# Performance work log

Measured on AMD Instinct MI355X. Metric: run time of the kernel, lower is better.

Reference implementation:

```python
import jax, jax.numpy as jnp
import numpy as np

B, T_DEC, T_ENC, E, ENC_D, VOCAB, SOS = 128, 550, 500, 512, 512, 31, 0


def setup_inputs() -> dict:
    key = jax.random.key(0)
    ks = jax.random.split(key, 16)
    s = 0.02
    d = {
        'encoder_output': jax.random.normal(ks[0], (B, T_ENC, ENC_D), jnp.float32),
        'emb': jax.random.normal(ks[1], (VOCAB, E), jnp.float32) * s,
        'w_ih0': jax.random.normal(ks[2], (4 * E, 2 * E), jnp.float32) * s,
        'w_hh0': jax.random.normal(ks[3], (4 * E, E), jnp.float32) * s,
        'b_ih0': jnp.zeros((4 * E,), jnp.float32),
        'b_hh0': jnp.zeros((4 * E,), jnp.float32),
        'w_ih1': jax.random.normal(ks[4], (4 * E, E), jnp.float32) * s,
        'w_hh1': jax.random.normal(ks[5], (4 * E, E), jnp.float32) * s,
        'b_ih1': jnp.zeros((4 * E,), jnp.float32),
        'b_hh1': jnp.zeros((4 * E,), jnp.float32),
        'wk': jax.random.normal(ks[6], (ENC_D, E), jnp.float32) * s,
        'wv': jax.random.normal(ks[7], (ENC_D, E), jnp.float32) * s,
        'w_o2c': jax.random.normal(ks[8], (E, 2 * E), jnp.float32) * s,
        'b_o2c': jnp.zeros((E,), jnp.float32),
        'b_cp': jnp.zeros((VOCAB,), jnp.float32),
    }
    return d


def _lstm_cell(x, h, c, w_ih, w_hh, b_ih, b_hh):
    # PyTorch LSTMCell gate order: i, f, g, o
    g = x @ w_ih.T + b_ih + h @ w_hh.T + b_hh
    i, f, gg, o = jnp.split(g, 4, axis=-1)
    c2 = jax.nn.sigmoid(f) * c + jax.nn.sigmoid(i) * jnp.tanh(gg)
    h2 = jax.nn.sigmoid(o) * jnp.tanh(c2)
    return h2, c2


def reference(encoder_output, emb, w_ih0, w_hh0, b_ih0, b_hh0,
              w_ih1, w_hh1, b_ih1, b_hh1, wk, wv, w_o2c, b_o2c, b_cp):
    # Precompute attention keys/values once (listener features are static)
    keys = jnp.einsum('bte,ed->btd', encoder_output, wk)    # [B,Tenc,E]
    values = jnp.einsum('bte,ed->btd', encoder_output, wv)  # [B,Tenc,E]

    z = jnp.zeros((B, E), jnp.float32)
    init = (z, z, z, z, z, jnp.full((B,), SOS, jnp.int32))

    def step(carry, _):
        h0, c0, h1, c1, ctx, sym = carry
        char_embed = emb[sym]                                # [B,E]
        x = jnp.concatenate([char_embed, ctx], axis=-1)      # [B,2E]
        h0, c0 = _lstm_cell(x, h0, c0, w_ih0, w_hh0, b_ih0, b_hh0)
        h1, c1 = _lstm_cell(h0, h1, c1, w_ih1, w_hh1, b_ih1, b_hh1)
        energy = jnp.einsum('btd,bd->bt', keys, h1)          # [B,Tenc]
        aw = jax.nn.softmax(energy, axis=-1)
        ctx = jnp.einsum('bt,btd->bd', aw, values)           # [B,E]
        cdn_in = jnp.concatenate([h1, ctx], axis=-1)         # [B,2E]
        hid = jax.nn.relu(cdn_in @ w_o2c.T + b_o2c)
        logits = hid @ emb.T + b_cp                          # [B,31] (tied weights)
        sym = jnp.argmax(logits, axis=-1).astype(jnp.int32)  # greedy feedback
        return (h0, c0, h1, c1, ctx, sym), (logits, aw)

    _, (raw, attn) = jax.lax.scan(step, init, None, length=T_DEC)
    # [T,B,...] -> [B,T,...]
    return jnp.transpose(raw, (1, 0, 2)), jnp.transpose(attn, (1, 0, 2))
```

## Files before the change

kernel.cpp:

```cpp
#include <hip/hip_runtime.h>
#include <math.h>

#define BATCH 128
#define TDEC  550
#define TENC  500
#define EDIM  512
#define VOC   31
#define NBLK  256
#define NTHR  512

#define OFF_WA   0u
#define OFF_WB   (OFF_WA + 2097152u)
#define OFF_GM   (OFF_WB + 2097152u)
#define OFF_E2G  (OFF_GM + 524288u)
#define OFF_BA   (OFF_E2G + 63488u)
#define OFF_BB   (OFF_BA + 2048u)
#define OFF_BG   (OFF_BB + 2048u)
#define OFF_ST   (OFF_BG + 512u)
#define OFF_H0T0 (OFF_ST   + 65536u)
#define OFF_H0T1 (OFF_H0T0 + 65536u)
#define OFF_H1T0 (OFF_H0T1 + 65536u)
#define OFF_H1T1 (OFF_H1T0 + 65536u)
#define OFF_C0T  (OFF_H1T1 + 65536u)
#define OFF_C1T  (OFF_C0T  + 65536u)
#define OFF_P    (OFF_C1T  + 65536u)
#define OFF_PL   (OFF_P    + 65536u)
#define OFF_PS   (OFF_PL   + 256u)
#define OFF_LB   (OFF_PS   + 131072u)
#define OFF_BAR  (OFF_LB   + 8192u)
#define OFF_WKT  (OFF_BAR  + 8192u)
#define OFF_H1BK (OFF_WKT  + 262144u)

typedef float f32x4_t __attribute__((ext_vector_type(4)));

__device__ __forceinline__ float ldv(const float* p) {
  return __hip_atomic_load((const float*)p, __ATOMIC_RELAXED, __HIP_MEMORY_SCOPE_AGENT);
}
__device__ __forceinline__ void stv(float* p, float v) {
  __hip_atomic_store(p, v, __ATOMIC_RELAXED, __HIP_MEMORY_SCOPE_AGENT);
}
__device__ __forceinline__ float4 ld_nt4(const float* p) {
  f32x4_t v = __builtin_nontemporal_load((const f32x4_t*)p);
  float4 r; r.x = v.x; r.y = v.y; r.z = v.z; r.w = v.w; return r;
}

__global__ void initCopy(const float* __restrict__ w_hh0, const float* __restrict__ w_ih1,
                         const float* __restrict__ w_hh1, const float* __restrict__ w_o2c,
                         const float* __restrict__ b_ih0, const float* __restrict__ b_hh0,
                         const float* __restrict__ b_ih1, const float* __restrict__ b_hh1,
                         const float* __restrict__ b_o2c, const float* __restrict__ wk,
                         float* __restrict__ ws)
{
  const unsigned n0 = 2048u*512u;
  const unsigned n1 = 2048u*512u;
  const unsigned n2 = 2048u*512u;
  const unsigned n3 = 512u*512u;
  const unsigned nz = 7u*65536u;
  const unsigned nw = 262144u;
  const unsigned NT = n0+n1+n2+n3 + 2048u+2048u+512u + nz + 8192u + 8192u + nw;
  for (unsigned i = blockIdx.x*blockDim.x + threadIdx.x; i < NT; i += gridDim.x*blockDim.x) {
    unsigned j = i;
    if (j < n0) { unsigned r = j & 2047u, k = j >> 11;
      ws[OFF_WA + (512u + k)*2048u + r] = w_hh0[(size_t)r*512u + k]; continue; }
    j -= n0;
    if (j < n1) { unsigned r = j & 2047u, k = j >> 11;
      ws[OFF_WB + k*2048u + r] = w_ih1[(size_t)r*512u + k]; continue; }
    j -= n1;
    if (j < n2) { unsigned r = j & 2047u, k = j >> 11;
      ws[OFF_WB + (512u + k)*2048u + r] = w_hh1[(size_t)r*512u + k]; continue; }
    j -= n2;
    if (j < n3) { unsigned r = j>>9, k = j&511u;
      ws[OFF_GM + r*1024u + k] = w_o2c[r*1024u + k]; continue; }
    j -= n3;
    if (j < 2048u) { ws[OFF_BA + j] = b_ih0[j] + b_hh0[j]; continue; }
    j -= 2048u;
    if (j < 2048u) { ws[OFF_BB + j] = b_ih1[j] + b_hh1[j]; continue; }
    j -= 2048u;
    if (j < 512u)  { ws[OFF_BG + j] = b_o2c[j]; continue; }
    j -= 512u;
    if (j < nz)    { ws[OFF_ST + j] = 0.f; continue; }
    j -= nz;
    if (j < 8192u) {
      unsigned buf = j>>12, v = j & 31u;
      ws[OFF_LB + j] = (buf==1u && v==0u) ? 1e9f : 0.f;
      continue; }
    j -= 8192u;
    if (j < 8192u) { ((unsigned*)(ws + OFF_BAR))[j] = 0u; continue; }
    j -= 8192u;
    { unsigned e = j>>9, d = j&511u;
      ws[OFF_WKT + j] = wk[d*512u + e]; }
  }
}

__global__ void initGemm(const float* __restrict__ w_ih0, const float* __restrict__ w_o2c,
                         const float* __restrict__ wvm, const float* __restrict__ emb,
                         float* __restrict__ ws)
{
  const unsigned n0 = 2048u*512u;
  const unsigned n1 = 512u*512u;
  const unsigned n2 = 31u*2048u;
  const unsigned NT = n0+n1+n2;
  for (unsigned i = blockIdx.x*blockDim.x + threadIdx.x; i < NT; i += gridDim.x*blockDim.x) {
    if (i < n0) {
      unsigned r = i & 2047u, d = i >> 11;
      const float* a = w_ih0 + (size_t)r*1024u + 512u;
      const float* b = wvm + (size_t)d*512u;
      float s = 0.f;
      for (int k = 0; k < 512; ++k) s = fmaf(a[k], b[k], s);
      ws[OFF_WA + d*2048u + r] = s;
    } else if (i < n0+n1) {
      unsigned j = i - n0; unsigned r = j>>9, d = j&511u;
      const float* a = w_o2c + (size_t)r*1024u + 512u;
      const float* b = wvm + (size_t)d*512u;
      float s = 0.f;
      for (int k = 0; k < 512; ++k) s = fmaf(a[k], b[k], s);
      ws[OFF_GM + r*1024u + 512u + d] = s;
    } else {
      unsigned j = i - n0 - n1; unsigned v = j>>11, g = j&2047u;
      const float* a = emb + (size_t)v*512u;
      const float* b = w_ih0 + (size_t)g*1024u;
      float s = 0.f;
      for (int k = 0; k < 512; ++k) s = fmaf(a[k], b[k], s);
      ws[OFF_E2G + v*2048u + g] = s;
    }
  }
}

__device__ __forceinline__ void groupbar(float* ws, int bg, int r5, unsigned tgt)
{
  unsigned* base = (unsigned*)(ws + OFF_BAR) + bg*1024;
  asm volatile("s_waitcnt vmcnt(0)" ::: "memory");
  __syncthreads();
  if (r5 == 0) {
    const int tid = threadIdx.x;
    if (tid > 0 && tid < 32) {
      unsigned* f = base + tid*16;
      while (__hip_atomic_load(f, __ATOMIC_RELAXED, __HIP_MEMORY_SCOPE_AGENT) < tgt)
        __builtin_amdgcn_s_sleep(2);
    }
    __syncthreads();
    if (tid == 0)
      __hip_atomic_store(base + 512, tgt, __ATOMIC_RELAXED, __HIP_MEMORY_SCOPE_AGENT);
    __syncthreads();
  } else {
    if (threadIdx.x == 0) {
      __hip_atomic_store(base + r5*16, tgt, __ATOMIC_RELAXED, __HIP_MEMORY_SCOPE_AGENT);
      while (__hip_atomic_load(base + 512, __ATOMIC_RELAXED, __HIP_MEMORY_SCOPE_AGENT) < tgt)
        __builtin_amdgcn_s_sleep(2);
    }
    __syncthreads();
  }
}

__device__ __forceinline__ float sigm(float x) { return 1.f/(1.f + expf(-x)); }

__launch_bounds__(NTHR)
__global__ void speller_main(const float* __restrict__ enc, const float* __restrict__ emb,
                             const float* __restrict__ wk,  const float* __restrict__ bcp,
                             float* __restrict__ ws, float* __restrict__ out)
{
  __shared__ __align__(16) float smem[15616];
  __shared__ unsigned long long amx[16];
  const int tid = threadIdx.x;
  const int blk = blockIdx.x;
  unsigned bstep = 0;

  float* rawout  = out;
  float* attnout = out + (size_t)BATCH*TDEC*VOC;

  const int r5  = blk & 31;
  const int hrg = (r5 & 7)*4 + (r5 >> 3);
  const int bg  = blk >> 5;
  const int bb0 = bg * 16;

  for (int t = 0; t < TDEC; ++t) {
    const int p = t & 1;
    float*       h0_cur  = ws + (p ? OFF_H0T1 : OFF_H0T0);
    const float* h0_prev = ws + (p ? OFF_H0T0 : OFF_H0T1);
    float*       h1_cur  = ws + (p ? OFF_H1T1 : OFF_H1T0);
    const float* h1_prev = ws + (p ? OFF_H1T0 : OFF_H1T1);

    {
      const float* Lb = ws + OFF_LB + (size_t)(p^1)*4096u;
      if (tid < 16) amx[tid] = 0ull;
      __syncthreads();
      if (hrg == 0 && t > 0 && tid < 496) {
        int bl = tid / 31, v = tid - bl*31;
        int bb = bb0 + bl;
        rawout[((size_t)bb*TDEC + (t-1))*VOC + v] = ldv(Lb + bb*32 + v) + bcp[v];
      }
      if (hrg == 1) {
        float* Lz = ws + OFF_LB + (size_t)p*4096u + (size_t)bb0*32u;
        if (tid < 512) stv(Lz + tid, 0.f);
      }
      if (tid < 496) {
        int bl = tid / 31, v = tid - bl*31;
        float f = ldv(Lb + (size_t)(bb0 + bl)*32u + v) + bcp[v];
        unsigned ub = __float_as_uint(f);
        ub = (ub & 0x80000000u) ? ~ub : (ub | 0x80000000u);
        unsigned long long key = ((unsigned long long)ub << 32) | (unsigned)(31 - v);
        atomicMax(&amx[bl], key);
      }
      const int gr = tid & 63, kh = tid >> 6;
      const int gi = gr >> 4, hp = gr & 15;
      const int j  = gi*512 + hrg*16 + hp;
      const float* wcol = ws + OFF_WA + j;
      float acc[16];
      #pragma unroll
      for (int b = 0; b < 16; ++b) acc[b] = 0.f;
      float* xs = smem;
      #pragma unroll 1
      for (int pass = 0; pass < 2; ++pass) {
        const float* src = pass ? h0_prev : (ws + OFF_ST);
        __syncthreads();
        float tmp[16];
        #pragma unroll
        for (int u = 0; u < 16; ++u) {
          int i = tid + u*512;
          tmp[u] = ldv(src + (size_t)(i >> 4)*128u + bb0 + (i & 15));
        }
        #pragma unroll
        for (int u = 0; u < 16; ++u) xs[tid + u*512] = tmp[u];
        __syncthreads();
        const int kb = kh * 64;
        #pragma unroll 8
        for (int kk = 0; kk < 64; ++kk) {
          float w = wcol[(size_t)(pass*512 + kb + kk)*2048u];
          const float* xr = xs + (size_t)(kb + kk)*16u;
          float4 x0 = *(const float4*)(xr);
          float4 x1 = *(const float4*)(xr + 4);
          float4 x2 = *(const float4*)(xr + 8);
          float4 x3 = *(const float4*)(xr + 12);
          acc[0]=fmaf(w,x0.x,acc[0]);  acc[1]=fmaf(w,x0.y,acc[1]);
          acc[2]=fmaf(w,x0.z,acc[2]);  acc[3]=fmaf(w,x0.w,acc[3]);
          acc[4]=fmaf(w,x1.x,acc[4]);  acc[5]=fmaf(w,x1.y,acc[5]);
          acc[6]=fmaf(w,x1.z,acc[6]);  acc[7]=fmaf(w,x1.w,acc[7]);
          acc[8]=fmaf(w,x2.x,acc[8]);  acc[9]=fmaf(w,x2.y,acc[9]);
          acc[10]=fmaf(w,x2.z,acc[10]); acc[11]=fmaf(w,x2.w,acc[11]);
          acc[12]=fmaf(w,x3.x,acc[12]); acc[13]=fmaf(w,x3.y,acc[13]);
          acc[14]=fmaf(w,x3.z,acc[14]); acc[15]=fmaf(w,x3.w,acc[15]);
        }
      }
      __syncthreads();
      float* part = smem;
      {
        float* pw = part + (size_t)gr*136u + kh*17;
        #pragma unroll
        for (int b = 0; b < 16; ++b) pw[b] = acc[b];
      }
      __syncthreads();
      if (tid < 256) {
        const int hp2 = tid >> 4, b2 = tid & 15;
        const int bb = bb0 + b2;
        const int j512 = hrg*16 + hp2;
        const int sy = 31 - (int)(amx[b2] & 31ull);
        float gv[4];
        #pragma unroll
        for (int g2 = 0; g2 < 4; ++g2) {
          const float* pr = part + (size_t)(g2*16 + hp2)*136u + b2;
          float s = 0.f;
          #pragma unroll
          for (int k2 = 0; k2 < 8; ++k2) s += pr[k2*17];
          s += (ws + OFF_E2G)[(size_t)sy*2048u + g2*512 + j512];
          s += (ws + OFF_BA)[g2*512 + j512];
          gv[g2] = s;
        }
        float ig = sigm(gv[0]), fg = sigm(gv[1]);
        float gg = tanhf(gv[2]), og = sigm(gv[3]);
        float* c0 = ws + OFF_C0T + (size_t)j512*128u + bb;
        float cold = *c0;
        float cnew = fg*cold + ig*gg;
        *c0 = cnew;
        stv(h0_cur + (size_t)j512*128u + bb, og*tanhf(cnew));
      }
    }
    groupbar(ws, bg, r5, ++bstep);

    {
      const int gr = tid & 63, kh = tid >> 6;
      const int gi = gr >> 4, hp = gr & 15;
      const int j  = gi*512 + hrg*16 + hp;
      const float* wcol = ws + OFF_WB + j;
      float acc[16];
      #pragma unroll
      for (int b = 0; b < 16; ++b) acc[b] = 0.f;
      float* xs = smem;
      #pragma unroll 1
      for (int pass = 0; pass < 2; ++pass) {
        const float* src = pass ? h1_prev : h0_cur;
        __syncthreads();
        float tmp[16];
        #pragma unroll
        for (int u = 0; u < 16; ++u) {
          int i = tid + u*512;
          tmp[u] = ldv(src + (size_t)(i >> 4)*128u + bb0 + (i & 15));
        }
        #pragma unroll
        for (int u = 0; u < 16; ++u) xs[tid + u*512] = tmp[u];
        __syncthreads();
        const int kb = kh * 64;
        #pragma unroll 8
        for (int kk = 0; kk < 64; ++kk) {
          float w = wcol[(size_t)(pass*512 + kb + kk)*2048u];
          const float* xr = xs + (size_t)(kb + kk)*16u;
          float4 x0 = *(const float4*)(xr);
          float4 x1 = *(const float4*)(xr + 4);
          float4 x2 = *(const float4*)(xr + 8);
          float4 x3 = *(const float4*)(xr + 12);
          acc[0]=fmaf(w,x0.x,acc[0]);  acc[1]=fmaf(w,x0.y,acc[1]);
          acc[2]=fmaf(w,x0.z,acc[2]);  acc[3]=fmaf(w,x0.w,acc[3]);
          acc[4]=fmaf(w,x1.x,acc[4]);  acc[5]=fmaf(w,x1.y,acc[5]);
          acc[6]=fmaf(w,x1.z,acc[6]);  acc[7]=fmaf(w,x1.w,acc[7]);
          acc[8]=fmaf(w,x2.x,acc[8]);  acc[9]=fmaf(w,x2.y,acc[9]);
          acc[10]=fmaf(w,x2.z,acc[10]); acc[11]=fmaf(w,x2.w,acc[11]);
          acc[12]=fmaf(w,x3.x,acc[12]); acc[13]=fmaf(w,x3.y,acc[13]);
          acc[14]=fmaf(w,x3.z,acc[14]); acc[15]=fmaf(w,x3.w,acc[15]);
        }
      }
      __syncthreads();
      float* part = smem;
      float* cellsL = smem + 8704;
      {
        float* pw = part + (size_t)gr*136u + kh*17;
        #pragma unroll
        for (int b = 0; b < 16; ++b) pw[b] = acc[b];
      }
      __syncthreads();
      if (tid < 256) {
        const int hp2 = tid >> 4, b2 = tid & 15;
        const int bb = bb0 + b2;
        const int j512 = hrg*16 + hp2;
        float gv[4];
        #pragma unroll
        for (int g2 = 0; g2 < 4; ++g2) {
          const float* pr = part + (size_t)(g2*16 + hp2)*136u + b2;
          float s = 0.f;
          #pragma unroll
          for (int k2 = 0; k2 < 8; ++k2) s += pr[k2*17];
          s += (ws + OFF_BB)[g2*512 + j512];
          gv[g2] = s;
        }
        float ig = sigm(gv[0]), fg = sigm(gv[1]);
        float gg = tanhf(gv[2]), og = sigm(gv[3]);
        float* c1 = ws + OFF_C1T + (size_t)j512*128u + bb;
        float cold = *c1;
        float cnew = fg*cold + ig*gg;
        *c1 = cnew;
        float hval = og*tanhf(cnew);
        stv(h1_cur + (size_t)j512*128u + bb, hval);
        cellsL[hp2*16 + b2] = hval;
      }
      __syncthreads();
      if (tid < 256) {
        const int b2 = tid >> 4, hp2 = tid & 15;
        stv(ws + OFF_H1BK + (size_t)(bb0 + b2)*512u + hrg*16 + hp2,
            cellsL[hp2*16 + b2]);
      }
    }
    groupbar(ws, bg, r5, ++bstep);

    {
      const int b = bb0 + (r5 >> 1), tau = r5 & 1;
      const int tbase = tau*250;
      float* tile = smem;
      float* qL   = smem + 13000;
      float* pL   = smem + 13520;
      float* sred = smem + 13568;
      float* h1L  = sred;

      if (tid < 128) {
        const float* hp = ws + OFF_H1BK + (size_t)b*512u + tid*4;
        float h0v = ldv(hp+0), h1v = ldv(hp+1), h2v = ldv(hp+2), h3v = ldv(hp+3);
        h1L[tid*4+0] = h0v; h1L[tid*4+1] = h1v;
        h1L[tid*4+2] = h2v; h1L[tid*4+3] = h3v;
      }
      __syncthreads();
      {
        const int eg = tid >> 7, dqq = (tid & 127)*4;
        const int e0 = eg*128;
        float4 qa = {0.f,0.f,0.f,0.f};
        const float* wkt = ws + OFF_WKT;
        for (int e = 0; e < 128; ++e) {
          float hv = h1L[e0 + e];
          float4 wv4 = *(const float4*)(wkt + (size_t)(e0+e)*512u + dqq);
          qa.x = fmaf(hv, wv4.x, qa.x); qa.y = fmaf(hv, wv4.y, qa.y);
          qa.z = fmaf(hv, wv4.z, qa.z); qa.w = fmaf(hv, wv4.w, qa.w);
        }
        *(float4*)(tile + eg*512 + dqq) = qa;
      }
      __syncthreads();
      if (tid < 128) {
        int dqq = tid*4;
        float4 a0 = *(float4*)(tile + dqq);
        float4 a1 = *(float4*)(tile + 512 + dqq);
        float4 a2 = *(float4*)(tile + 1024 + dqq);
        float4 a3 = *(float4*)(tile + 1536 + dqq);
        float4 q4;
        q4.x = a0.x+a1.x+a2.x+a3.x; q4.y = a0.y+a1.y+a2.y+a3.y;
        q4.z = a0.z+a1.z+a2.z+a3.z; q4.w = a0.w+a1.w+a2.w+a3.w;
        *(float4*)(qL + dqq) = q4;
      }
      float4 rv[7];
      const float* encb = enc + ((size_t)b*TENC + tbase)*EDIM;
      #pragma unroll
      for (int jj = 0; jj < 7; ++jj) {
        int i2 = tid + jj*512;
        if (i2 < 3200) rv[jj] = ld_nt4(encb + (size_t)i2*4u);
      }
      float sa0=0.f, sa1=0.f, sa2=0.f, sa3=0.f;
      float ltot = 0.f;
      const int rr = tid >> 3, cc = tid & 7;
      const int qr = tid >> 7, dqq = (tid & 127)*4;
      const int rs = qr*6 + (qr>0 ? 1 : 0);
      const int rcnt = (qr==0) ? 7 : 6;
      __syncthreads();
      for (int ti = 0; ti < 10; ++ti) {
        #pragma unroll
        for (int jj = 0; jj < 7; ++jj) {
          int i2 = tid + jj*512;
          if (i2 < 3200) { int r = i2 >> 7, c = i2 & 127; *(float4*)(tile + r*520 + c*4) = rv[jj]; }
        }
        __syncthreads();
        if (ti < 9) {
          const float* encn = encb + (size_t)(ti+1)*25u*EDIM;
          #pragma unroll
          for (int jj = 0; jj < 7; ++jj) {
            int i2 = tid + jj*512;
            if (i2 < 3200) rv[jj] = ld_nt4(encn + (size_t)i2*4u);
          }
        }
        if (rr < 25) {
          float a = 0.f;
          const float* tr = tile + rr*520;
          #pragma unroll
          for (int i = 0; i < 16; ++i) {
            int d = i*32 + cc*4;
            float4 tv = *(const float4*)(tr + d);
            float4 qv = *(const float4*)(qL + d);
            a = fmaf(tv.x,qv.x,a); a = fmaf(tv.y,qv.y,a);
            a = fmaf(tv.z,qv.z,a); a = fmaf(tv.w,qv.w,a);
          }
          a += __shfl_xor(a, 1); a += __shfl_xor(a, 2); a += __shfl_xor(a, 4);
          if (cc == 0) {
            float pv = expf(a);
            pL[rr] = pv;
            stv(ws + OFF_P + (size_t)b*512u + tbase + ti*25 + rr, pv);
          }
        }
        __syncthreads();
        if (tid < 32) {
          float pv = (tid < 25) ? pL[tid] : 0.f;
          pv += __shfl_xor(pv, 1); pv += __shfl_xor(pv, 2); pv += __shfl_xor(pv, 4);
          pv += __shfl_xor(pv, 8); pv += __shfl_xor(pv, 16);
          if (tid == 0) ltot += pv;
        }
        {
          const float* tb = tile + dqq;
          for (int r = rs; r < rs + rcnt; ++r) {
            float w = pL[r];
            float4 tv = *(const float4*)(tb + r*520);
            sa0 = fmaf(w, tv.x, sa0); sa1 = fmaf(w, tv.y, sa1);
            sa2 = fmaf(w, tv.z, sa2); sa3 = fmaf(w, tv.w, sa3);
          }
        }
        __syncthreads();
      }
      {
        float4 sv; sv.x = sa0; sv.y = sa1; sv.z = sa2; sv.w = sa3;
        *(float4*)(sred + qr*512 + dqq) = sv;
      }
      __syncthreads();
      if (tid < 128) {
        int d4 = tid*4;
        float4 s0 = *(float4*)(sred + d4);
        float4 s1 = *(float4*)(sred + 512 + d4);
        float4 s2 = *(float4*)(sred + 1024 + d4);
        float4 s3 = *(float4*)(sred + 1536 + d4);
        float* pd = ws + OFF_PS + (size_t)(b*2 + tau)*512u + d4;
        stv(pd+0, s0.x+s1.x+s2.x+s3.x);
        stv(pd+1, s0.y+s1.y+s2.y+s3.y);
        stv(pd+2, s0.z+s1.z+s2.z+s3.z);
        stv(pd+3, s0.w+s1.w+s2.w+s3.w);
      }
      if (tid == 0) stv(ws + OFF_PL + b*2 + tau, ltot);
    }
    groupbar(ws, bg, r5, ++bstep);

    {
      const int bh = r5 >> 4, it = r5 & 15;
      const int b0 = bb0 + bh*8, i0 = it*32;
      float* xo   = smem;
      float* scsL = smem + 8256;
      float* hidP = smem + 8264;
      float* hidL = smem + 8776;
      if (tid < 8) {
        int bb = b0 + tid;
        float l0 = ldv(ws + OFF_PL + bb*2);
        float l1 = ldv(ws + OFF_PL + bb*2 + 1);
        scsL[tid] = 1.f / (l0 + l1);
      }
      __syncthreads();
      for (int i = tid; i < 1024; i += NTHR) {
        int bl = i >> 7, kq = (i & 127)*4;
        const float* hp = ws + OFF_H1BK + (size_t)(b0+bl)*512u + kq;
        float h0v = ldv(hp+0), h1v = ldv(hp+1), h2v = ldv(hp+2), h3v = ldv(hp+3);
        xo[bl*1032 + kq+0] = h0v; xo[bl*1032 + kq+1] = h1v;
        xo[bl*1032 + kq+2] = h2v; xo[bl*1032 + kq+3] = h3v;
      }
      for (int i = tid; i < 1024; i += NTHR) {
        int bl = i >> 7, dq2 = (i & 127)*4;
        const float* psd = ws + OFF_PS + (size_t)(b0 + bl)*2u*512u;
        float a0 = ldv(psd + dq2+0), a1 = ldv(psd + dq2+1);
        float a2 = ldv(psd + dq2+2), a3 = ldv(psd + dq2+3);
        float b0v = ldv(psd + 512 + dq2+0), b1v = ldv(psd + 512 + dq2+1);
        float b2v = ldv(psd + 512 + dq2+2), b3v = ldv(psd + 512 + dq2+3);
        float sc = scsL[bl];
        xo[bl*1032 + 512 + dq2+0] = (a0+b0v)*sc;
        xo[bl*1032 + 512 + dq2+1] = (a1+b1v)*sc;
        xo[bl*1032 + 512 + dq2+2] = (a2+b2v)*sc;
        xo[bl*1032 + 512 + dq2+3] = (a3+b3v)*sc;
      }
      __syncthreads();
      {
        const int bl = tid & 7, il = (tid >> 3) & 31, kh = tid >> 8;
        float a = 0.f;
        const float4* Gr = (const float4*)(ws + OFF_GM + (size_t)(i0 + il)*1024u + kh*512);
        const float4* xr = (const float4*)(xo + bl*1032 + kh*512);
        for (int k2 = 0; k2 < 128; ++k2) {
          float4 g = Gr[k2], x = xr[k2];
          a = fmaf(g.x,x.x,a); a = fmaf(g.y,x.y,a);
          a = fmaf(g.z,x.z,a); a = fmaf(g.w,x.w,a);
        }
        hidP[(kh << 8) + (tid & 255)] = a;
      }
      __syncthreads();
      if (tid < 256) {
        int bl = tid & 7, il = tid >> 3;
        float h = hidP[tid] + hidP[256 + tid] + (ws + OFF_BG)[i0 + il];
        hidL[bl*33 + il] = fmaxf(h, 0.f);
      }
      if (it == 0) {
        for (int i = tid; i < 1000; i += NTHR) {
          int bl = i / 125, f = i - bl*125;
          int bb = b0 + bl;
          const float* pp = ws + OFF_P + (size_t)bb*512u + f*4;
          float p0v = ldv(pp+0), p1v = ldv(pp+1), p2v = ldv(pp+2), p3v = ldv(pp+3);
          float sc = scsL[bl];
          float4 v; v.x = p0v*sc; v.y = p1v*sc; v.z = p2v*sc; v.w = p3v*sc;
          *(float4*)(attnout + ((size_t)bb*TDEC + t)*TENC + f*4) = v;
        }
        for (int i = tid; i < 4096; i += NTHR) {
          int bl = i & 7, d = i >> 3;
          stv(ws + OFF_ST + (size_t)d*128 + b0 + bl, xo[bl*1032 + 512 + d]);
        }
      }
      __syncthreads();
      if (tid < 248) {
        int bl = tid & 7, v = tid >> 3;
        float s = 0.f;
        const float* er = emb + (size_t)v*512u + i0;
        const float* hrow = hidL + bl*33;
        #pragma unroll
        for (int ii = 0; ii < 32; ++ii) s = fmaf(hrow[ii], er[ii], s);
        float* Lw = ws + OFF_LB + (size_t)p*4096u;
        atomicAdd(&Lw[(b0 + bl)*32 + v], s);
      }
    }
    groupbar(ws, bg, r5, ++bstep);
  }

  if (hrg == 0 && tid < 496) {
    const float* Lb = ws + OFF_LB + 4096u;
    int bl = tid / 31, v = tid - bl*31;
    int bb = bb0 + bl;
    rawout[((size_t)bb*TDEC + (TDEC-1))*VOC + v] = ldv(Lb + bb*32 + v) + bcp[v];
  }
}

extern "C" void kernel_launch(void* const* d_in, const int* in_sizes, int n_in,
                              void* d_out, int out_size, void* d_ws, size_t ws_size,
                              hipStream_t stream)
{
  (void)in_sizes; (void)n_in; (void)out_size; (void)ws_size;
  const float* enc   = (const float*)d_in[0];
  const float* emb   = (const float*)d_in[1];
  const float* w_ih0 = (const float*)d_in[2];
  const float* w_hh0 = (const float*)d_in[3];
  const float* b_ih0 = (const float*)d_in[4];
  const float* b_hh0 = (const float*)d_in[5];
  const float* w_ih1 = (const float*)d_in[6];
  const float* w_hh1 = (const float*)d_in[7];
  const float* b_ih1 = (const float*)d_in[8];
  const float* b_hh1 = (const float*)d_in[9];
  const float* wk    = (const float*)d_in[10];
  const float* wvm   = (const float*)d_in[11];
  const float* w_o2c = (const float*)d_in[12];
  const float* b_o2c = (const float*)d_in[13];
  const float* bcp   = (const float*)d_in[14];
  float* ws   = (float*)d_ws;
  float* outp = (float*)d_out;

  initCopy<<<2048, 256, 0, stream>>>(w_hh0, w_ih1, w_hh1, w_o2c,
                                     b_ih0, b_hh0, b_ih1, b_hh1, b_o2c, wk, ws);
  initGemm<<<2048, 256, 0, stream>>>(w_ih0, w_o2c, wvm, emb, ws);
  speller_main<<<NBLK, NTHR, 0, stream>>>(enc, emb, wk, bcp, ws, outp);
}
```

Baseline: 74.95 ms.

## Double persistent block count by halving batch rows per barrier group

The launch goes from 256 to 512 persistent blocks. Each barrier group now owns 8 batch rows instead of 16, and the LSTM, attention and output-projection stages are re-indexed to match. The goal is shorter per-step latency in the recurrent loop by spreading the per-step work over more CUs and waves. In exchange, each block still streams the same weight columns for half the batch, so total weight traffic through cache doubles. All 512 blocks must also be co-resident for the spin barriers, and half the blocks sit idle during the attention stage.

```diff
diff --git a/kernel.cpp b/kernel.cpp
--- a/kernel.cpp
+++ b/kernel.cpp
@@ -6,7 +6,7 @@
 #define TENC  500
 #define EDIM  512
 #define VOC   31
-#define NBLK  256
+#define NBLK  512
 #define NTHR  512
 
 #define OFF_WA   0u
@@ -128,7 +128,7 @@
 
 __device__ __forceinline__ void groupbar(float* ws, int bg, int r5, unsigned tgt)
 {
-  unsigned* base = (unsigned*)(ws + OFF_BAR) + bg*1024;
+  unsigned* base = (unsigned*)(ws + OFF_BAR) + bg*512;
   asm volatile("s_waitcnt vmcnt(0)" ::: "memory");
   __syncthreads();
   if (r5 == 0) {
@@ -140,12 +140,12 @@
     }
     __syncthreads();
     if (tid == 0)
-      __hip_atomic_store(base + 512, tgt, __ATOMIC_RELAXED, __HIP_MEMORY_SCOPE_AGENT);
+      __hip_atomic_store(base + 511, tgt, __ATOMIC_RELAXED, __HIP_MEMORY_SCOPE_AGENT);
     __syncthreads();
   } else {
     if (threadIdx.x == 0) {
       __hip_atomic_store(base + r5*16, tgt, __ATOMIC_RELAXED, __HIP_MEMORY_SCOPE_AGENT);
-      while (__hip_atomic_load(base + 512, __ATOMIC_RELAXED, __HIP_MEMORY_SCOPE_AGENT) < tgt)
+      while (__hip_atomic_load(base + 511, __ATOMIC_RELAXED, __HIP_MEMORY_SCOPE_AGENT) < tgt)
         __builtin_amdgcn_s_sleep(2);
     }
     __syncthreads();
@@ -154,13 +154,13 @@
 
 __device__ __forceinline__ float sigm(float x) { return 1.f/(1.f + expf(-x)); }
 
-__launch_bounds__(NTHR)
+__launch_bounds__(NTHR, 4)
 __global__ void speller_main(const float* __restrict__ enc, const float* __restrict__ emb,
                              const float* __restrict__ wk,  const float* __restrict__ bcp,
                              float* __restrict__ ws, float* __restrict__ out)
 {
   __shared__ __align__(16) float smem[15616];
-  __shared__ unsigned long long amx[16];
+  __shared__ unsigned long long amx[8];
   const int tid = threadIdx.x;
   const int blk = blockIdx.x;
   unsigned bstep = 0;
@@ -171,7 +171,7 @@
   const int r5  = blk & 31;
   const int hrg = (r5 & 7)*4 + (r5 >> 3);
   const int bg  = blk >> 5;
-  const int bb0 = bg * 16;
+  const int bb0 = bg * 8;
 
   for (int t = 0; t < TDEC; ++t) {
     const int p = t & 1;
@@ -182,18 +182,18 @@
 
     {
       const float* Lb = ws + OFF_LB + (size_t)(p^1)*4096u;
-      if (tid < 16) amx[tid] = 0ull;
-      __syncthreads();
-      if (hrg == 0 && t > 0 && tid < 496) {
+      if (tid < 8) amx[tid] = 0ull;
+      __syncthreads();
+      if (r5 == 0 && t > 0 && tid < 248) {
         int bl = tid / 31, v = tid - bl*31;
         int bb = bb0 + bl;
         rawout[((size_t)bb*TDEC + (t-1))*VOC + v] = ldv(Lb + bb*32 + v) + bcp[v];
       }
       if (hrg == 1) {
         float* Lz = ws + OFF_LB + (size_t)p*4096u + (size_t)bb0*32u;
-        if (tid < 512) stv(Lz + tid, 0.f);
-      }
-      if (tid < 496) {
+        if (tid < 256) stv(Lz + tid, 0.f);
+      }
+      if (tid < 248) {
         int bl = tid / 31, v = tid - bl*31;
         float f = ldv(Lb + (size_t)(bb0 + bl)*32u + v) + bcp[v];
         unsigned ub = __float_as_uint(f);
@@ -205,62 +205,56 @@
       const int gi = gr >> 4, hp = gr & 15;
       const int j  = gi*512 + hrg*16 + hp;
       const float* wcol = ws + OFF_WA + j;
-      float acc[16];
+      float acc[8];
       #pragma unroll
-      for (int b = 0; b < 16; ++b) acc[b] = 0.f;
+      for (int b = 0; b < 8; ++b) acc[b] = 0.f;
       float* xs = smem;
       #pragma unroll 1
       for (int pass = 0; pass < 2; ++pass) {
         const float* src = pass ? h0_prev : (ws + OFF_ST);
         __syncthreads();
-        float tmp[16];
-        #pragma unroll
-        for (int u = 0; u < 16; ++u) {
+        float tmp[8];
+        #pragma unroll
+        for (int u = 0; u < 8; ++u) {
           int i = tid + u*512;
-          tmp[u] = ldv(src + (size_t)(i >> 4)*128u + bb0 + (i & 15));
-        }
-        #pragma unroll
-        for (int u = 0; u < 16; ++u) xs[tid + u*512] = tmp[u];
+          tmp[u] = ldv(src + (size_t)(i >> 3)*128u + bb0 + (i & 7));
+        }
+        #pragma unroll
+        for (int u = 0; u < 8; ++u) xs[tid + u*512] = tmp[u];
         __syncthreads();
         const int kb = kh * 64;
         #pragma unroll 8
         for (int kk = 0; kk < 64; ++kk) {
           float w = wcol[(size_t)(pass*512 + kb + kk)*2048u];
-          const float* xr = xs + (size_t)(kb + kk)*16u;
+          const float* xr = xs + (size_t)(kb + kk)*8u;
           float4 x0 = *(const float4*)(xr);
           float4 x1 = *(const float4*)(xr + 4);
-          float4 x2 = *(const float4*)(xr + 8);
-          float4 x3 = *(const float4*)(xr + 12);
-          acc[0]=fmaf(w,x0.x,acc[0]);  acc[1]=fmaf(w,x0.y,acc[1]);
-          acc[2]=fmaf(w,x0.z,acc[2]);  acc[3]=fmaf(w,x0.w,acc[3]);
-          acc[4]=fmaf(w,x1.x,acc[4]);  acc[5]=fmaf(w,x1.y,acc[5]);
-          acc[6]=fmaf(w,x1.z,acc[6]);  acc[7]=fmaf(w,x1.w,acc[7]);
-          acc[8]=fmaf(w,x2.x,acc[8]);  acc[9]=fmaf(w,x2.y,acc[9]);
-          acc[10]=fmaf(w,x2.z,acc[10]); acc[11]=fmaf(w,x2.w,acc[11]);
-          acc[12]=fmaf(w,x3.x,acc[12]); acc[13]=fmaf(w,x3.y,acc[13]);
-          acc[14]=fmaf(w,x3.z,acc[14]); acc[15]=fmaf(w,x3.w,acc[15]);
+          acc[0]=fmaf(w,x0.x,acc[0]); acc[1]=fmaf(w,x0.y,acc[1]);
+          acc[2]=fmaf(w,x0.z,acc[2]); acc[3]=fmaf(w,x0.w,acc[3]);
+          acc[4]=fmaf(w,x1.x,acc[4]); acc[5]=fmaf(w,x1.y,acc[5]);
+          acc[6]=fmaf(w,x1.z,acc[6]); acc[7]=fmaf(w,x1.w,acc[7]);
         }
       }
       __syncthreads();
       float* part = smem;
       {
-        float* pw = part + (size_t)gr*136u + kh*17;
-        #pragma unroll
-        for (int b = 0; b < 16; ++b) pw[b] = acc[b];
-      }
-      __syncthreads();
-      if (tid < 256) {
-        const int hp2 = tid >> 4, b2 = tid & 15;
+        float* pw = part + (size_t)gr*72u + kh*9;
+        #pragma unroll
+        for (int b = 0; b < 8; ++b) pw[b] = acc[b];
+      }
+      __syncthreads();
+      if (tid < 128) {
+        const int hp2 = tid >> 3, b2 = tid & 7;
         const int bb = bb0 + b2;
         const int j512 = hrg*16 + hp2;
         const int sy = 31 - (int)(amx[b2] & 31ull);
         float gv[4];
         #pragma unroll
         for (int g2 = 0; g2 < 4; ++g2) {
-          const float* pr = part + (size_t)(g2*16 + hp2)*136u + b2;
+          const float* pr = part + (size_t)(g2*16 + hp2)*72u + b2;
           float s = 0.f;
           #pragma unroll
-          for (int k2 = 0; k2 < 8; ++k2) s += pr[k2*17];
+          for (int k2 = 0; k2 < 8; ++k2) s += pr[k2*9];
           s += (ws + OFF_E2G)[(size_t)sy*2048u + g2*512 + j512];
           s += (ws + OFF_BA)[g2*512 + j512];
           gv[g2] = s;
@@ -281,62 +275,56 @@
       const int gi = gr >> 4, hp = gr & 15;
       const int j  = gi*512 + hrg*16 + hp;
       const float* wcol = ws + OFF_WB + j;
-      float acc[16];
+      float acc[8];
       #pragma unroll
-      for (int b = 0; b < 16; ++b) acc[b] = 0.f;
+      for (int b = 0; b < 8; ++b) acc[b] = 0.f;
       float* xs = smem;
       #pragma unroll 1
       for (int pass = 0; pass < 2; ++pass) {
         const float* src = pass ? h1_prev : h0_cur;
         __syncthreads();
-        float tmp[16];
-        #pragma unroll
-        for (int u = 0; u < 16; ++u) {
+        float tmp[8];
+        #pragma unroll
+        for (int u = 0; u < 8; ++u) {
           int i = tid + u*512;
-          tmp[u] = ldv(src + (size_t)(i >> 4)*128u + bb0 + (i & 15));
-        }
-        #pragma unroll
-        for (int u = 0; u < 16; ++u) xs[tid + u*512] = tmp[u];
+          tmp[u] = ldv(src + (size_t)(i >> 3)*128u + bb0 + (i & 7));
+        }
+        #pragma unroll
+        for (int u = 0; u < 8; ++u) xs[tid + u*512] = tmp[u];
         __syncthreads();
         const int kb = kh * 64;
         #pragma unroll 8
         for (int kk = 0; kk < 64; ++kk) {
           float w = wcol[(size_t)(pass*512 + kb + kk)*2048u];
-          const float* xr = xs + (size_t)(kb + kk)*16u;
+          const float* xr = xs + (size_t)(kb + kk)*8u;
           float4 x0 = *(const float4*)(xr);
           float4 x1 = *(const float4*)(xr + 4);
-          float4 x2 = *(const float4*)(xr + 8);
-          float4 x3 = *(const float4*)(xr + 12);
-          acc[0]=fmaf(w,x0.x,acc[0]);  acc[1]=fmaf(w,x0.y,acc[1]);
-          acc[2]=fmaf(w,x0.z,acc[2]);  acc[3]=fmaf(w,x0.w,acc[3]);
-          acc[4]=fmaf(w,x1.x,acc[4]);  acc[5]=fmaf(w,x1.y,acc[5]);
-          acc[6]=fmaf(w,x1.z,acc[6]);  acc[7]=fmaf(w,x1.w,acc[7]);
-          acc[8]=fmaf(w,x2.x,acc[8]);  acc[9]=fmaf(w,x2.y,acc[9]);
-          acc[10]=fmaf(w,x2.z,acc[10]); acc[11]=fmaf(w,x2.w,acc[11]);
-          acc[12]=fmaf(w,x3.x,acc[12]); acc[13]=fmaf(w,x3.y,acc[13]);
-          acc[14]=fmaf(w,x3.z,acc[14]); acc[15]=fmaf(w,x3.w,acc[15]);
-        }
-      }
-      __syncthreads();
-      float* part = smem;
-      float* cellsL = smem + 8704;
-      {
-        float* pw = part + (size_t)gr*136u + kh*17;
-        #pragma unroll
-        for (int b = 0; b < 16; ++b) pw[b] = acc[b];
-      }
-      __syncthreads();
-      if (tid < 256) {
-        const int hp2 = tid >> 4, b2 = tid & 15;
+          acc[0]=fmaf(w,x0.x,acc[0]); acc[1]=fmaf(w,x0.y,acc[1]);
+          acc[2]=fmaf(w,x0.z,acc[2]); acc[3]=fmaf(w,x0.w,acc[3]);
+          acc[4]=fmaf(w,x1.x,acc[4]); acc[5]=fmaf(w,x1.y,acc[5]);
+          acc[6]=fmaf(w,x1.z,acc[6]); acc[7]=fmaf(w,x1.w,acc[7]);
+        }
+      }
+      __syncthreads();
+      float* part   = smem;
+      float* cellsL = smem + 4608;
+      {
+        float* pw = part + (size_t)gr*72u + kh*9;
+        #pragma unroll
+        for (int b = 0; b < 8; ++b) pw[b] = acc[b];
+      }
+      __syncthreads();
+      if (tid < 128) {
+        const int hp2 = tid >> 3, b2 = tid & 7;
         const int bb = bb0 + b2;
         const int j512 = hrg*16 + hp2;
         float gv[4];
         #pragma unroll
         for (int g2 = 0; g2 < 4; ++g2) {
-          const float* pr = part + (size_t)(g2*16 + hp2)*136u + b2;
+          const float* pr = part + (size_t)(g2*16 + hp2)*72u + b2;
           float s = 0.f;
           #pragma unroll
-          for (int k2 = 0; k2 < 8; ++k2) s += pr[k2*17];
+          for (int k2 = 0; k2 < 8; ++k2) s += pr[k2*9];
           s += (ws + OFF_BB)[g2*512 + j512];
           gv[g2] = s;
         }
@@ -348,18 +336,18 @@
         *c1 = cnew;
         float hval = og*tanhf(cnew);
         stv(h1_cur + (size_t)j512*128u + bb, hval);
-        cellsL[hp2*16 + b2] = hval;
-      }
-      __syncthreads();
-      if (tid < 256) {
+        cellsL[hp2*8 + b2] = hval;
+      }
+      __syncthreads();
+      if (tid < 128) {
         const int b2 = tid >> 4, hp2 = tid & 15;
         stv(ws + OFF_H1BK + (size_t)(bb0 + b2)*512u + hrg*16 + hp2,
-            cellsL[hp2*16 + b2]);
+            cellsL[hp2*8 + b2]);
       }
     }
     groupbar(ws, bg, r5, ++bstep);
 
-    {
+    if (r5 < 16) {
       const int b = bb0 + (r5 >> 1), tau = r5 & 1;
       const int tbase = tau*250;
       float* tile = smem;
@@ -488,32 +476,33 @@
 
     {
       const int bh = r5 >> 4, it = r5 & 15;
-      const int b0 = bb0 + bh*8, i0 = it*32;
+      const int b0 = bb0 + bh*4, i0 = it*32;
       float* xo   = smem;
-      float* scsL = smem + 8256;
-      float* hidP = smem + 8264;
-      float* hidL = smem + 8776;
-      if (tid < 8) {
+      float* scsL = smem + 4128;
+      float* hidP = smem + 4136;
+      float* hidL = smem + 4648;
+      if (tid < 4) {
         int bb = b0 + tid;
         float l0 = ldv(ws + OFF_PL + bb*2);
         float l1 = ldv(ws + OFF_PL + bb*2 + 1);
         scsL[tid] = 1.f / (l0 + l1);
       }
       __syncthreads();
-      for (int i = tid; i < 1024; i += NTHR) {
-        int bl = i >> 7, kq = (i & 127)*4;
+      {
+        int bl = tid >> 7, kq = (tid & 127)*4;
         const float* hp = ws + OFF_H1BK + (size_t)(b0+bl)*512u + kq;
         float h0v = ldv(hp+0), h1v = ldv(hp+1), h2v = ldv(hp+2), h3v = ldv(hp+3);
         xo[bl*1032 + kq+0] = h0v; xo[bl*1032 + kq+1] = h1v;
         xo[bl*1032 + kq+2] = h2v; xo[bl*1032 + kq+3] = h3v;
       }
-      for (int i = tid; i < 1024; i += NTHR) {
-        int bl = i >> 7, dq2 = (i & 127)*4;
+      {
+        int bl = tid >> 7, dq2 = (tid & 127)*4;
         const float* psd = ws + OFF_PS + (size_t)(b0 + bl)*2u*512u;
         float a0 = ldv(psd + dq2+0), a1 = ldv(psd + dq2+1);
         float a2 = ldv(psd + dq2+2), a3 = ldv(psd + dq2+3);
         float b0v = ldv(psd + 512 + dq2+0), b1v = ldv(psd + 512 + dq2+1);
         float b2v = ldv(psd + 512 + dq2+2), b3v = ldv(psd + 512 + dq2+3);
+        __syncthreads();
         float sc = scsL[bl];
         xo[bl*1032 + 512 + dq2+0] = (a0+b0v)*sc;
         xo[bl*1032 + 512 + dq2+1] = (a1+b1v)*sc;
@@ -522,26 +511,27 @@
       }
       __syncthreads();
       {
-        const int bl = tid & 7, il = (tid >> 3) & 31, kh = tid >> 8;
+        const int bl = tid & 3, il = (tid >> 2) & 31, kh = tid >> 7;
         float a = 0.f;
-        const float4* Gr = (const float4*)(ws + OFF_GM + (size_t)(i0 + il)*1024u + kh*512);
-        const float4* xr = (const float4*)(xo + bl*1032 + kh*512);
-        for (int k2 = 0; k2 < 128; ++k2) {
+        const float4* Gr = (const float4*)(ws + OFF_GM + (size_t)(i0 + il)*1024u + kh*256);
+        const float4* xr = (const float4*)(xo + bl*1032 + kh*256);
+        for (int k2 = 0; k2 < 64; ++k2) {
           float4 g = Gr[k2], x = xr[k2];
           a = fmaf(g.x,x.x,a); a = fmaf(g.y,x.y,a);
           a = fmaf(g.z,x.z,a); a = fmaf(g.w,x.w,a);
         }
-        hidP[(kh << 8) + (tid & 255)] = a;
-      }
-      __syncthreads();
-      if (tid < 256) {
-        int bl = tid & 7, il = tid >> 3;
-        float h = hidP[tid] + hidP[256 + tid] + (ws + OFF_BG)[i0 + il];
+        hidP[(kh << 7) + (tid & 127)] = a;
+      }
+      __syncthreads();
+      if (tid < 128) {
+        int bl = tid & 3, il = tid >> 2;
+        float h = hidP[tid] + hidP[128 + tid] + hidP[256 + tid] + hidP[384 + tid]
+                + (ws + OFF_BG)[i0 + il];
         hidL[bl*33 + il] = fmaxf(h, 0.f);
       }
       if (it == 0) {
-        for (int i = tid; i < 1000; i += NTHR) {
-          int bl = i / 125, f = i - bl*125;
+        if (tid < 500) {
+          int bl = tid / 125, f = tid - bl*125;
           int bb = b0 + bl;
           const float* pp = ws + OFF_P + (size_t)bb*512u + f*4;
           float p0v = ldv(pp+0), p1v = ldv(pp+1), p2v = ldv(pp+2), p3v = ldv(pp+3);
@@ -549,14 +539,14 @@
           float4 v; v.x = p0v*sc; v.y = p1v*sc; v.z = p2v*sc; v.w = p3v*sc;
           *(float4*)(attnout + ((size_t)bb*TDEC + t)*TENC + f*4) = v;
         }
-        for (int i = tid; i < 4096; i += NTHR) {
-          int bl = i & 7, d = i >> 3;
+        for (int i = tid; i < 2048; i += NTHR) {
+          int bl = i & 3, d = i >> 2;
           stv(ws + OFF_ST + (size_t)d*128 + b0 + bl, xo[bl*1032 + 512 + d]);
         }
       }
       __syncthreads();
-      if (tid < 248) {
-        int bl = tid & 7, v = tid >> 3;
+      if (tid < 124) {
+        int bl = tid & 3, v = tid >> 2;
         float s = 0.f;
         const float* er = emb + (size_t)v*512u + i0;
         const float* hrow = hidL + bl*33;
@@ -569,7 +559,7 @@
     groupbar(ws, bg, r5, ++bstep);
   }
 
-  if (hrg == 0 && tid < 496) {
+  if (r5 == 0 && tid < 248) {
     const float* Lb = ws + OFF_LB + 4096u;
     int bl = tid / 31, v = tid - bl*31;
     int bb = bb0 + bl;
```

New measurement: 93.88 ms. +25.3%, slower.
